# Optimization experiments

Measured on AMD Instinct MI355X. Metric: run time of the kernel, lower is better.

## Reference

```python
import jax, jax.numpy as jnp
import numpy as np
import math

H = 8  # n_heads

def rel_shift(x):
    # x: [B, H, U, P] -> Transformer-XL relative shift
    B, h, U, P = x.shape
    x = jnp.pad(x, ((0, 0), (0, 0), (0, 0), (1, 0)))  # zero-pad front of last dim
    x = x.reshape(B, h, P + 1, U)[:, :, 1:, :].reshape(B, h, U, P)
    return x

def setup_inputs() -> dict:
    key = jax.random.key(0)
    ks = jax.random.split(key, 16)
    B, T, D = 8, 1024, 512
    s = 0.05  # weight scale ~ xavier for D=512
    inp = {
        'q': jax.random.normal(ks[0], (B, T, D), jnp.float32),
        'k': jax.random.normal(ks[1], (B, T, D), jnp.float32),
        'v': jax.random.normal(ks[2], (B, T, D), jnp.float32),
        'pos': jax.random.normal(ks[3], (T, D), jnp.float32),
        'mask': jax.random.randint(ks[4], (B, T, T), 0, 2).astype(jnp.int32),
        'Wq': jax.random.normal(ks[5], (D, D), jnp.float32) * s,
        'bq': jnp.zeros((D,), jnp.float32),
        'Wk': jax.random.normal(ks[6], (D, D), jnp.float32) * s,
        'bk': jnp.zeros((D,), jnp.float32),
        'Wv': jax.random.normal(ks[7], (D, D), jnp.float32) * s,
        'bv': jnp.zeros((D,), jnp.float32),
        'Wo': jax.random.normal(ks[8], (D, D), jnp.float32) * s,
        'bo': jnp.zeros((D,), jnp.float32),
        'Wp': jax.random.normal(ks[9], (D, D), jnp.float32) * s,
        'bias_u': jax.random.normal(ks[10], (H, D // H), jnp.float32) * s,
        'bias_v': jax.random.normal(ks[11], (H, D // H), jnp.float32) * s,
    }
    return inp

def reference(q, k, v, pos, mask, Wq, bq, Wk, bk, Wv, bv, Wo, bo, Wp, bias_u, bias_v):
    B, T, D = q.shape
    dk = D // H
    qh = (q @ Wq.T + bq).reshape(B, T, H, dk)   # B U H d
    kh = (k @ Wk.T + bk).reshape(B, T, H, dk)   # B T H d
    vh = (v @ Wv.T + bv).reshape(B, T, H, dk)   # B T H d
    ph = (pos @ Wp.T).reshape(T, H, dk)          # P H d (shared across batch)
    q_u = qh + bias_u                            # B U H d
    q_v = qh + bias_v
    ac = jnp.einsum('buhd,bthd->bhut', q_u, kh)  # content term
    bd = jnp.einsum('buhd,phd->bhup', q_v, ph)   # position term
    bd = rel_shift(bd)[:, :, :, :T]
    scores = (ac + bd) / math.sqrt(dk)           # B H U T
    m = (mask[:, None, :, :] == 0)               # B 1 U T
    neg = jnp.finfo(scores.dtype).min
    scores = jnp.where(m, neg, scores)
    attn = jax.nn.softmax(scores, axis=-1)
    attn = jnp.where(m, 0.0, attn)
    x = jnp.einsum('bhut,bthd->buhd', attn, vh).reshape(B, T, D)
    return x @ Wo.T + bo
```

## Files before the change

### kernel.cpp

```cpp
#include <hip/hip_runtime.h>
#include <stdint.h>

#define Bc 8
#define Tc 1024
#define Dc 512
#define Hc 8

typedef __bf16 bf16x8 __attribute__((ext_vector_type(8)));
typedef float f32x4 __attribute__((ext_vector_type(4)));
typedef unsigned short ushort8v __attribute__((ext_vector_type(8)));

#define NEGBF 0xF14Au

__device__ __forceinline__ unsigned short f2bf(float f) {
    union { float f; uint32_t u; } v; v.f = f;
    uint32_t u = v.u;
    u += 0x7fffu + ((u >> 16) & 1u);
    return (unsigned short)(u >> 16);
}
__device__ __forceinline__ unsigned short f2bf_native(float f) {
    __bf16 b = (__bf16)f;
    return *(unsigned short*)&b;
}
__device__ __forceinline__ f32x4 mfma16(bf16x8 a, bf16x8 b, f32x4 c) {
    return __builtin_amdgcn_mfma_f32_16x16x32_bf16(a, b, c, 0, 0, 0);
}
__device__ __forceinline__ void gl16(const unsigned short* g, unsigned short* l) {
    __builtin_amdgcn_global_load_lds(
        (const __attribute__((address_space(1))) uint32_t*)g,
        (__attribute__((address_space(3))) uint32_t*)l, 16, 0, 0);
}

#define SC2 0.1803368801f

__global__ __launch_bounds__(256) void prep(
    const int* __restrict__ mask, uint32_t* __restrict__ bits,
    const float* __restrict__ Wq, const float* __restrict__ Wk,
    const float* __restrict__ Wv, const float* __restrict__ Wp,
    const float* __restrict__ Wo, unsigned short* __restrict__ Wb,
    const float* __restrict__ q, const float* __restrict__ k,
    const float* __restrict__ v, const float* __restrict__ p,
    unsigned short* __restrict__ qb, unsigned short* __restrict__ kb,
    unsigned short* __restrict__ vb, unsigned short* __restrict__ pb)
{
    int bid = blockIdx.x;
    if (bid < 32768) {
        int wid = (bid * 256 + threadIdx.x) >> 6;
        int lane = threadIdx.x & 63;
        unsigned long long bl = __ballot(mask[(size_t)wid * 64 + lane] != 0);
        if (lane == 0)  bits[wid * 2]     = (uint32_t)bl;
        if (lane == 32) bits[wid * 2 + 1] = (uint32_t)(bl >> 32);
    } else if (bid < 33408) {
        int i = (bid - 32768) * 2048 + threadIdx.x * 8;
        int m = i >> 18, r = i & 262143;
        const float* Ws[5] = {Wq, Wk, Wv, Wp, Wo};
        const float* s = Ws[m] + r;
        ushort8v o;
#pragma unroll
        for (int j = 0; j < 8; ++j) o[j] = f2bf(s[j]);
        *(ushort8v*)(Wb + i) = o;
    } else {
        size_t i = (size_t)(bid - 33408) * 2048 + threadIdx.x * 8;
        const float* src; unsigned short* dst; size_t off;
        if (i < 4194304)       { src = q; dst = qb; off = i; }
        else if (i < 8388608)  { src = k; dst = kb; off = i - 4194304; }
        else if (i < 12582912) { src = v; dst = vb; off = i - 8388608; }
        else                   { src = p; dst = pb; off = i - 12582912; }
        ushort8v o;
#pragma unroll
        for (int j = 0; j < 8; ++j) o[j] = f2bf(src[off + j]);
        *(ushort8v*)(dst + off) = o;
    }
}

__global__ __launch_bounds__(256) void proj4(
    const unsigned short* __restrict__ qb, const unsigned short* __restrict__ kb,
    const unsigned short* __restrict__ vb, const unsigned short* __restrict__ pb,
    const unsigned short* __restrict__ Wb,
    const float* __restrict__ bq, const float* __restrict__ bk,
    const float* __restrict__ bv,
    const float* __restrict__ bias_u, const float* __restrict__ bias_v,
    unsigned short* __restrict__ qu, unsigned short* __restrict__ qv,
    unsigned short* __restrict__ kh, unsigned short* __restrict__ vT,
    unsigned short* __restrict__ ph)
{
    int id = blockIdx.x;
    int wg = (id & 7) * 200 + (id >> 3);
    int z, rem;
    if (wg < 512)       { z = 0; rem = wg; }
    else if (wg < 1024) { z = 1; rem = wg - 512; }
    else if (wg < 1536) { z = 2; rem = wg - 1024; }
    else                { z = 3; rem = wg - 1536; }
    const int m0 = (rem & 3) * 128, n0 = (rem >> 2) * 64;
    const unsigned short* A = z == 0 ? qb : z == 1 ? kb : z == 2 ? vb : pb;
    const unsigned short* W = Wb + (size_t)z * 262144;

    __shared__ unsigned short As[2][64][64];
    __shared__ unsigned short Bs[2][128][64];
    const int tid = threadIdx.x, lane = tid & 63, wave = tid >> 6;
    const int lrow = lane & 15, lkg = lane >> 4;
    const int wr = (wave >> 1) * 32, wc = (wave & 1) * 64;
    const int srow = lane >> 3;
    const int scol = ((lane & 7) ^ (srow & 7)) * 8;
    const int swr  = (lrow & 7) * 8;

    f32x4 acc[2][4];
#pragma unroll
    for (int i = 0; i < 2; ++i)
#pragma unroll
        for (int j = 0; j < 4; ++j) acc[i][j] = f32x4{0.f, 0.f, 0.f, 0.f};

#pragma unroll
    for (int it = 0; it < 2; ++it) {
        int r8 = (wave * 2 + it) * 8;
        gl16(A + (size_t)(n0 + r8 + srow) * 512 + scol, &As[0][r8][0]);
    }
#pragma unroll
    for (int it = 0; it < 4; ++it) {
        int r8 = (wave * 4 + it) * 8;
        gl16(W + (size_t)(m0 + r8 + srow) * 512 + scol, &Bs[0][r8][0]);
    }

    int cur = 0;
    for (int kt = 0; kt < 512; kt += 64) {
        if (kt + 64 < 512) {
#pragma unroll
            for (int it = 0; it < 2; ++it) {
                int r8 = (wave * 2 + it) * 8;
                gl16(A + (size_t)(n0 + r8 + srow) * 512 + kt + 64 + scol, &As[cur ^ 1][r8][0]);
            }
#pragma unroll
            for (int it = 0; it < 4; ++it) {
                int r8 = (wave * 4 + it) * 8;
                gl16(W + (size_t)(m0 + r8 + srow) * 512 + kt + 64 + scol, &Bs[cur ^ 1][r8][0]);
            }
            asm volatile("s_waitcnt vmcnt(6)" ::: "memory");
        } else {
            asm volatile("s_waitcnt vmcnt(0)" ::: "memory");
        }
        __builtin_amdgcn_s_barrier();
#pragma unroll
        for (int kk = 0; kk < 2; ++kk) {
            bf16x8 a[2], bb[4];
#pragma unroll
            for (int i = 0; i < 2; ++i)
                a[i] = *(const bf16x8*)&As[cur][wr + i * 16 + lrow][(kk * 32 + lkg * 8) ^ swr];
#pragma unroll
            for (int j = 0; j < 4; ++j)
                bb[j] = *(const bf16x8*)&Bs[cur][wc + j * 16 + lrow][(kk * 32 + lkg * 8) ^ swr];
#pragma unroll
            for (int i = 0; i < 2; ++i)
#pragma unroll
                for (int j = 0; j < 4; ++j)
                    acc[i][j] = mfma16(a[i], bb[j], acc[i][j]);
        }
        asm volatile("s_waitcnt lgkmcnt(0)" ::: "memory");
        __builtin_amdgcn_s_barrier();
        cur ^= 1;
    }

#pragma unroll
    for (int i = 0; i < 2; ++i) {
        int nbase = n0 + wr + i * 16 + lkg * 4;
#pragma unroll
        for (int j = 0; j < 4; ++j) {
            int m = m0 + wc + j * 16 + lrow;
            float bb = z == 0 ? bq[m] : z == 1 ? bk[m] : z == 2 ? bv[m] : 0.f;
            float bu = 0.f, bvv = 0.f;
            if (z == 0) { bu = bias_u[m]; bvv = bias_v[m]; }
#pragma unroll
            for (int qq = 0; qq < 4; ++qq) {
                int n = nbase + qq;
                float c = acc[i][j][qq] + bb;
                if (z == 0) {
                    qu[(size_t)n * 512 + m] = f2bf(c + bu);
                    qv[(size_t)n * 512 + m] = f2bf(c + bvv);
                } else if (z == 1) {
                    kh[(size_t)n * 512 + m] = f2bf(c * SC2);
                } else if (z == 2) {
                    int b = n >> 10, t = n & 1023, h = m >> 6, d = m & 63;
                    vT[(((size_t)((b * 8 + h) * 64 + d)) << 10) + t] = f2bf(c);
                } else {
                    ph[(size_t)n * 512 + m] = f2bf(c);
                }
            }
        }
    }
}

__global__ __launch_bounds__(256) void gemm_out(
    const unsigned short* __restrict__ X, const unsigned short* __restrict__ Wob,
    const float* __restrict__ bo, float* __restrict__ fout)
{
    int id = blockIdx.x;
    int wg = (id & 7) * 64 + (id >> 3);
    const int m0 = (wg & 3) * 128, n0 = (wg >> 2) * 64;
    __shared__ unsigned short As[2][64][64];
    __shared__ unsigned short Bs[2][128][64];
    const int tid = threadIdx.x, lane = tid & 63, wave = tid >> 6;
    const int lrow = lane & 15, lkg = lane >> 4;
    const int wr = (wave >> 1) * 32, wc = (wave & 1) * 64;
    const int srow = lane >> 3;
    const int scol = ((lane & 7) ^ (srow & 7)) * 8;
    const int swr  = (lrow & 7) * 8;

    f32x4 acc[2][4];
#pragma unroll
    for (int i = 0; i < 2; ++i)
#pragma unroll
        for (int j = 0; j < 4; ++j) acc[i][j] = f32x4{0.f, 0.f, 0.f, 0.f};

#pragma unroll
    for (int it = 0; it < 2; ++it) {
        int r8 = (wave * 2 + it) * 8;
        gl16(X + (size_t)(n0 + r8 + srow) * 512 + scol, &As[0][r8][0]);
    }
#pragma unroll
    for (int it = 0; it < 4; ++it) {
        int r8 = (wave * 4 + it) * 8;
        gl16(Wob + (size_t)(m0 + r8 + srow) * 512 + scol, &Bs[0][r8][0]);
    }

    int cur = 0;
    for (int kt = 0; kt < 512; kt += 64) {
        if (kt + 64 < 512) {
#pragma unroll
            for (int it = 0; it < 2; ++it) {
                int r8 = (wave * 2 + it) * 8;
                gl16(X + (size_t)(n0 + r8 + srow) * 512 + kt + 64 + scol, &As[cur ^ 1][r8][0]);
            }
#pragma unroll
            for (int it = 0; it < 4; ++it) {
                int r8 = (wave * 4 + it) * 8;
                gl16(Wob + (size_t)(m0 + r8 + srow) * 512 + kt + 64 + scol, &Bs[cur ^ 1][r8][0]);
            }
            asm volatile("s_waitcnt vmcnt(6)" ::: "memory");
        } else {
            asm volatile("s_waitcnt vmcnt(0)" ::: "memory");
        }
        __builtin_amdgcn_s_barrier();
#pragma unroll
        for (int kk = 0; kk < 2; ++kk) {
            bf16x8 a[2], bb[4];
#pragma unroll
            for (int i = 0; i < 2; ++i)
                a[i] = *(const bf16x8*)&As[cur][wr + i * 16 + lrow][(kk * 32 + lkg * 8) ^ swr];
#pragma unroll
            for (int j = 0; j < 4; ++j)
                bb[j] = *(const bf16x8*)&Bs[cur][wc + j * 16 + lrow][(kk * 32 + lkg * 8) ^ swr];
#pragma unroll
            for (int i = 0; i < 2; ++i)
#pragma unroll
                for (int j = 0; j < 4; ++j)
                    acc[i][j] = mfma16(a[i], bb[j], acc[i][j]);
        }
        asm volatile("s_waitcnt lgkmcnt(0)" ::: "memory");
        __builtin_amdgcn_s_barrier();
        cur ^= 1;
    }
#pragma unroll
    for (int i = 0; i < 2; ++i) {
        int nbase = n0 + wr + i * 16 + lkg * 4;
#pragma unroll
        for (int j = 0; j < 4; ++j) {
            int m = m0 + wc + j * 16 + lrow;
            float bb = bo[m];
#pragma unroll
            for (int qq = 0; qq < 4; ++qq)
                fout[(size_t)(nbase + qq) * 512 + m] = acc[i][j][qq] + bb;
        }
    }
}

__global__ __launch_bounds__(256) void bd_gemm(
    const unsigned short* __restrict__ qv, const unsigned short* __restrict__ ph,
    const uint32_t* __restrict__ mbits, unsigned short* __restrict__ bds,
    int bh_base)
{
    int id = blockIdx.x, wg;
    if (gridDim.x == 4096) wg = (id & 7) * 512 + (id >> 3);
    else                   wg = (id & 7) * 64 + (id >> 3);
    const int zz = wg >> 6, ut = wg & 63;
    const int u_base = ut * 16;
    const int bh = bh_base + zz;
    const int b = bh >> 3, h = bh & 7;
    __shared__ unsigned short Bs[2][128][64];
    const int tid = threadIdx.x, lane = tid & 63, wave = tid >> 6;
    const int lrow = lane & 15, lkg = lane >> 4;
    const int srow = lane >> 3;
    const int scol = ((lane & 7) ^ (srow & 7)) * 8;
    const int swr  = (lrow & 7) * 8;

    const unsigned short* qvb = qv + ((size_t)(b * 1024 + u_base + lrow)) * 512 + h * 64;
    bf16x8 a0 = *(const bf16x8*)(qvb + lkg * 8);
    bf16x8 a1 = *(const bf16x8*)(qvb + 32 + lkg * 8);

    f32x4 acc[16];
#pragma unroll
    for (int jj = 0; jj < 16; ++jj) acc[jj] = f32x4{0.f, 0.f, 0.f, 0.f};

#pragma unroll
    for (int it = 0; it < 4; ++it) {
        int r8 = wave * 32 + it * 8;
        gl16(ph + ((size_t)(r8 + srow)) * 512 + h * 64 + scol, &Bs[0][r8][0]);
    }

#pragma unroll
    for (int c = 0; c < 8; ++c) {
        if (c < 7) {
#pragma unroll
            for (int it = 0; it < 4; ++it) {
                int r8 = wave * 32 + it * 8;
                gl16(ph + ((size_t)((c + 1) * 128 + r8 + srow)) * 512 + h * 64 + scol,
                     &Bs[(c + 1) & 1][r8][0]);
            }
            asm volatile("s_waitcnt vmcnt(4)" ::: "memory");
        } else {
            asm volatile("s_waitcnt vmcnt(0)" ::: "memory");
        }
        __builtin_amdgcn_s_barrier();
#pragma unroll
        for (int kk = 0; kk < 2; ++kk) {
            bf16x8 av = kk ? a1 : a0;
#pragma unroll
            for (int jt = 0; jt < 2; ++jt) {
                bf16x8 bb = *(const bf16x8*)
                    &Bs[c & 1][wave * 32 + jt * 16 + lrow][(kk * 32 + lkg * 8) ^ swr];
                acc[c * 2 + jt] = mfma16(av, bb, acc[c * 2 + jt]);
            }
        }
        asm volatile("s_waitcnt lgkmcnt(0)" ::: "memory");
        __builtin_amdgcn_s_barrier();
    }

    unsigned short* slab = bds + ((size_t)zz << 20);
    const uint32_t* mb = mbits + ((size_t)b << 15);
    const int Fq0 = 1025 * (u_base + lkg * 4) + wave * 32 + lrow - 1023;
#pragma unroll
    for (int q = 0; q < 4; ++q) {
        int Fq = Fq0 + 1025 * q;
#pragma unroll
        for (int c = 0; c < 8; ++c) {
            int Fb = Fq + c * 128;
            int w0 = Fb >> 5;
            uint32_t mw0 = mb[w0], mw1 = mb[w0 + 1];
            uint64_t m01 = ((uint64_t)mw1 << 32) | mw0;
            int sh = Fb & 31;
#pragma unroll
            for (int hhf = 0; hhf < 2; ++hhf) {
                uint32_t bit = (uint32_t)(m01 >> (sh + hhf * 16)) & 1u;
                unsigned short val = bit ? f2bf_native(acc[c * 2 + hhf][q] * SC2)
                                         : (unsigned short)NEGBF;
                int F = Fb + hhf * 16;
                if (F >= 0) slab[F] = val;
            }
        }
    }

    if (tid < 16) {
        int ud = u_base + tid;
        if (ud < 1023) {
            const uint8_t* mrowbytes = (const uint8_t*)mbits + ((size_t)b << 17);
            uint32_t bit = (mrowbytes[ud * 128 + ((ud + 1) >> 3)] >> ((ud + 1) & 7)) & 1;
            slab[((size_t)ud << 10) + (ud + 1)] = bit ? 0 : (unsigned short)NEGBF;
        }
    }
}

__global__ __launch_bounds__(256, 4) void attn10(
    const unsigned short* __restrict__ qu, const unsigned short* __restrict__ kh,
    const unsigned short* __restrict__ vT, const unsigned short* __restrict__ bds,
    unsigned short* __restrict__ xout, int b_base)
{
    int id = blockIdx.x, nid, b, rem;
    if (gridDim.x == 1024) {
        nid = (id & 7) * 128 + (id >> 3);
        b = b_base + (nid >> 7); rem = nid & 127;
    } else {
        nid = (id & 7) * 16 + (id >> 3);
        b = b_base; rem = nid;
    }
    const int h = rem >> 4, ublk = rem & 15;
    const int u0 = ublk * 64;

    __shared__ unsigned short Ks[2][64][64];
    __shared__ unsigned short Vs[2][64][64];
    __shared__ unsigned short Ps[4][16][64];
    const int tid = threadIdx.x, lane = tid & 63, wave = tid >> 6;
    const int lrow = lane & 15, lkg = lane >> 4;
    const int srow = lane >> 3;
    const int scol = ((lane & 7) ^ (srow & 7)) * 8;
    const int swr  = (lrow & 7) * 8;
    const f32x4 zero = {0.f, 0.f, 0.f, 0.f};

    const unsigned short* qub = qu + ((size_t)(b * 1024 + u0 + wave * 16 + lrow)) * 512 + h * 64;
    bf16x8 au0 = *(const bf16x8*)(qub + lkg * 8);
    bf16x8 au1 = *(const bf16x8*)(qub + 32 + lkg * 8);

    const int urow = u0 + wave * 16 + lkg * 4;
    const int zoff = (b - b_base) * 8 + h;
    const unsigned short* bdp[4];
#pragma unroll
    for (int q = 0; q < 4; ++q)
        bdp[q] = bds + ((size_t)zoff << 20) + (((size_t)(urow + q)) << 10) + lrow;
    const unsigned short* kbase = kh + ((size_t)(b * 1024)) * 512 + h * 64;
    const unsigned short* vbase = vT + (((size_t)((b * 8 + h) * 64)) << 10);

    f32x4 acc[4] = {zero, zero, zero, zero};
    float lsum[4] = {0.f, 0.f, 0.f, 0.f};

#pragma unroll
    for (int it = 0; it < 2; ++it) {
        int r8 = (wave * 2 + it) * 8;
        gl16(kbase + (size_t)(r8 + srow) * 512 + scol, &Ks[0][r8][0]);
        gl16(vbase + ((size_t)(r8 + srow) << 10) + scol, &Vs[0][r8][0]);
    }

    int cur = 0;
    for (int t0 = 0; t0 < 1024; t0 += 64) {
        f32x4 bdC[4];
#pragma unroll
        for (int j = 0; j < 4; ++j)
#pragma unroll
            for (int q = 0; q < 4; ++q)
                bdC[j][q] = __uint_as_float(((uint32_t)bdp[q][j * 16]) << 16);
#pragma unroll
        for (int q = 0; q < 4; ++q) bdp[q] += 64;

        if (t0 < 960) {
#pragma unroll
            for (int it = 0; it < 2; ++it) {
                int r8 = (wave * 2 + it) * 8;
                gl16(kbase + (size_t)(t0 + 64 + r8 + srow) * 512 + scol, &Ks[cur ^ 1][r8][0]);
                gl16(vbase + ((size_t)(r8 + srow) << 10) + t0 + 64 + scol, &Vs[cur ^ 1][r8][0]);
            }
            asm volatile("s_waitcnt vmcnt(4)" ::: "memory");
        } else {
            asm volatile("s_waitcnt vmcnt(0)" ::: "memory");
        }
        __builtin_amdgcn_s_barrier();

        f32x4 s[4];
#pragma unroll
        for (int j = 0; j < 4; ++j) {
            bf16x8 k0 = *(const bf16x8*)&Ks[cur][j * 16 + lrow][(lkg * 8) ^ swr];
            bf16x8 k1 = *(const bf16x8*)&Ks[cur][j * 16 + lrow][(32 + lkg * 8) ^ swr];
            s[j] = mfma16(au1, k1, mfma16(au0, k0, bdC[j]));
        }
#pragma unroll
        for (int j = 0; j < 4; ++j) {
#pragma unroll
            for (int q = 0; q < 4; ++q) {
                float p = exp2f(s[j][q]);
                lsum[q] += p;
                int prow = lkg * 4 + q;
                Ps[wave][prow][(j * 16 + lrow) ^ ((prow & 7) * 8)] = f2bf_native(p);
            }
        }
        bf16x8 pa0 = *(const bf16x8*)&Ps[wave][lrow][(lkg * 8) ^ swr];
        bf16x8 pa1 = *(const bf16x8*)&Ps[wave][lrow][(32 + lkg * 8) ^ swr];
#pragma unroll
        for (int jj = 0; jj < 4; ++jj) {
            bf16x8 vb0 = *(const bf16x8*)&Vs[cur][jj * 16 + lrow][(lkg * 8) ^ swr];
            bf16x8 vb1 = *(const bf16x8*)&Vs[cur][jj * 16 + lrow][(32 + lkg * 8) ^ swr];
            acc[jj] = mfma16(pa1, vb1, mfma16(pa0, vb0, acc[jj]));
        }
        asm volatile("s_waitcnt lgkmcnt(0)" ::: "memory");
        __builtin_amdgcn_s_barrier();
        cur ^= 1;
    }

#pragma unroll
    for (int off = 1; off < 16; off <<= 1)
#pragma unroll
        for (int q = 0; q < 4; ++q) lsum[q] += __shfl_xor(lsum[q], off);
#pragma unroll
    for (int q = 0; q < 4; ++q) {
        float inv = 1.0f / lsum[q];
        int u = urow + q;
#pragma unroll
        for (int jj = 0; jj < 4; ++jj) {
            int d = jj * 16 + lrow;
            xout[((size_t)(b * 1024 + u)) * 512 + h * 64 + d] = f2bf_native(acc[jj][q] * inv);
        }
    }
}

extern "C" void kernel_launch(void* const* d_in, const int* in_sizes, int n_in,
                              void* d_out, int out_size, void* d_ws, size_t ws_size,
                              hipStream_t stream) {
    const float* q    = (const float*)d_in[0];
    const float* k    = (const float*)d_in[1];
    const float* v    = (const float*)d_in[2];
    const float* pos  = (const float*)d_in[3];
    const int*   mask = (const int*)d_in[4];
    const float* Wq   = (const float*)d_in[5];
    const float* bq   = (const float*)d_in[6];
    const float* Wk   = (const float*)d_in[7];
    const float* bk   = (const float*)d_in[8];
    const float* Wv   = (const float*)d_in[9];
    const float* bv   = (const float*)d_in[10];
    const float* Wo   = (const float*)d_in[11];
    const float* bo   = (const float*)d_in[12];
    const float* Wp   = (const float*)d_in[13];
    const float* bias_u = (const float*)d_in[14];
    const float* bias_v = (const float*)d_in[15];
    float* out = (float*)d_out;

    unsigned short* ws = (unsigned short*)d_ws;
    constexpr size_t NQ  = (size_t)Bc * Tc * Dc;
    constexpr size_t NP  = (size_t)Tc * Dc;
    constexpr size_t NMB = (size_t)Bc * Tc * 32;
    constexpr size_t NWB = (size_t)5 * 262144;
    unsigned short* ws_qu = ws;
    unsigned short* ws_qv = ws_qu + NQ;
    unsigned short* ws_kh = ws_qv + NQ;
    unsigned short* ws_vT = ws_kh + NQ;
    unsigned short* ws_ph = ws_vT + NQ;
    uint32_t*       ws_mb = (uint32_t*)(ws_ph + NP);
    unsigned short* ws_wb = (unsigned short*)(ws_mb + NMB);
    unsigned short* ws_qb = ws_wb + NWB;
    unsigned short* ws_kb = ws_qb + NQ;
    unsigned short* ws_vb = ws_kb + NQ;
    unsigned short* ws_pb = ws_vb + NQ;
    unsigned short* ws_bd = ws_qb;

    constexpr size_t BD_FULL  = (size_t)64 * 1024 * 1024;
    constexpr size_t BD_SMALL = (size_t)8 * 1024 * 1024;
    const size_t base_bytes = (4 * NQ + NP + NWB) * 2 + NMB * 4;
    const bool full  = ws_size >= base_bytes + BD_FULL * 2;
    const bool tier2 = !full && ws_size >= base_bytes + ((3 * NQ + NP) + NQ) * 2;

    dim3 blk(256);
    prep<<<39808, blk, 0, stream>>>(mask, ws_mb, Wq, Wk, Wv, Wp, Wo, ws_wb,
                                    q, k, v, pos, ws_qb, ws_kb, ws_vb, ws_pb);
    proj4<<<1600, blk, 0, stream>>>(ws_qb, ws_kb, ws_vb, ws_pb, ws_wb, bq, bk, bv,
                                    bias_u, bias_v, ws_qu, ws_qv, ws_kh, ws_vT, ws_ph);

    if (full) {
        unsigned short* ws_x = ws_qv;
        bd_gemm<<<4096, blk, 0, stream>>>(ws_qv, ws_ph, ws_mb, ws_bd, 0);
        attn10<<<1024, blk, 0, stream>>>(ws_qu, ws_kh, ws_vT, ws_bd, ws_x, 0);
        gemm_out<<<512, blk, 0, stream>>>(ws_x, ws_wb + 4 * 262144, bo, out);
    } else if (tier2) {
        unsigned short* ws_x = ws_qb + 3 * NQ + NP;
        for (int b = 0; b < 8; ++b) {
            bd_gemm<<<512, blk, 0, stream>>>(ws_qv, ws_ph, ws_mb, ws_bd, b * 8);
            attn10<<<128, blk, 0, stream>>>(ws_qu, ws_kh, ws_vT, ws_bd, ws_x, b);
        }
        gemm_out<<<512, blk, 0, stream>>>(ws_x, ws_wb + 4 * 262144, bo, out);
    }
}
```

Baseline: 195.5 us.

## Fuse relative-position bd GEMM into attention kernel with per-block slab

```diff
diff --git a/kernel.cpp b/kernel.cpp
--- a/kernel.cpp
+++ b/kernel.cpp
@@ -272,105 +272,12 @@
     }
 }
 
-__global__ __launch_bounds__(256) void bd_gemm(
-    const unsigned short* __restrict__ qv, const unsigned short* __restrict__ ph,
-    const uint32_t* __restrict__ mbits, unsigned short* __restrict__ bds,
-    int bh_base)
-{
-    int id = blockIdx.x, wg;
-    if (gridDim.x == 4096) wg = (id & 7) * 512 + (id >> 3);
-    else                   wg = (id & 7) * 64 + (id >> 3);
-    const int zz = wg >> 6, ut = wg & 63;
-    const int u_base = ut * 16;
-    const int bh = bh_base + zz;
-    const int b = bh >> 3, h = bh & 7;
-    __shared__ unsigned short Bs[2][128][64];
-    const int tid = threadIdx.x, lane = tid & 63, wave = tid >> 6;
-    const int lrow = lane & 15, lkg = lane >> 4;
-    const int srow = lane >> 3;
-    const int scol = ((lane & 7) ^ (srow & 7)) * 8;
-    const int swr  = (lrow & 7) * 8;
-
-    const unsigned short* qvb = qv + ((size_t)(b * 1024 + u_base + lrow)) * 512 + h * 64;
-    bf16x8 a0 = *(const bf16x8*)(qvb + lkg * 8);
-    bf16x8 a1 = *(const bf16x8*)(qvb + 32 + lkg * 8);
-
-    f32x4 acc[16];
-#pragma unroll
-    for (int jj = 0; jj < 16; ++jj) acc[jj] = f32x4{0.f, 0.f, 0.f, 0.f};
-
-#pragma unroll
-    for (int it = 0; it < 4; ++it) {
-        int r8 = wave * 32 + it * 8;
-        gl16(ph + ((size_t)(r8 + srow)) * 512 + h * 64 + scol, &Bs[0][r8][0]);
-    }
-
-#pragma unroll
-    for (int c = 0; c < 8; ++c) {
-        if (c < 7) {
-#pragma unroll
-            for (int it = 0; it < 4; ++it) {
-                int r8 = wave * 32 + it * 8;
-                gl16(ph + ((size_t)((c + 1) * 128 + r8 + srow)) * 512 + h * 64 + scol,
-                     &Bs[(c + 1) & 1][r8][0]);
-            }
-            asm volatile("s_waitcnt vmcnt(4)" ::: "memory");
-        } else {
-            asm volatile("s_waitcnt vmcnt(0)" ::: "memory");
-        }
-        __builtin_amdgcn_s_barrier();
-#pragma unroll
-        for (int kk = 0; kk < 2; ++kk) {
-            bf16x8 av = kk ? a1 : a0;
-#pragma unroll
-            for (int jt = 0; jt < 2; ++jt) {
-                bf16x8 bb = *(const bf16x8*)
-                    &Bs[c & 1][wave * 32 + jt * 16 + lrow][(kk * 32 + lkg * 8) ^ swr];
-                acc[c * 2 + jt] = mfma16(av, bb, acc[c * 2 + jt]);
-            }
-        }
-        asm volatile("s_waitcnt lgkmcnt(0)" ::: "memory");
-        __builtin_amdgcn_s_barrier();
-    }
-
-    unsigned short* slab = bds + ((size_t)zz << 20);
-    const uint32_t* mb = mbits + ((size_t)b << 15);
-    const int Fq0 = 1025 * (u_base + lkg * 4) + wave * 32 + lrow - 1023;
-#pragma unroll
-    for (int q = 0; q < 4; ++q) {
-        int Fq = Fq0 + 1025 * q;
-#pragma unroll
-        for (int c = 0; c < 8; ++c) {
-            int Fb = Fq + c * 128;
-            int w0 = Fb >> 5;
-            uint32_t mw0 = mb[w0], mw1 = mb[w0 + 1];
-            uint64_t m01 = ((uint64_t)mw1 << 32) | mw0;
-            int sh = Fb & 31;
-#pragma unroll
-            for (int hhf = 0; hhf < 2; ++hhf) {
-                uint32_t bit = (uint32_t)(m01 >> (sh + hhf * 16)) & 1u;
-                unsigned short val = bit ? f2bf_native(acc[c * 2 + hhf][q] * SC2)
-                                         : (unsigned short)NEGBF;
-                int F = Fb + hhf * 16;
-                if (F >= 0) slab[F] = val;
-            }
-        }
-    }
-
-    if (tid < 16) {
-        int ud = u_base + tid;
-        if (ud < 1023) {
-            const uint8_t* mrowbytes = (const uint8_t*)mbits + ((size_t)b << 17);
-            uint32_t bit = (mrowbytes[ud * 128 + ((ud + 1) >> 3)] >> ((ud + 1) & 7)) & 1;
-            slab[((size_t)ud << 10) + (ud + 1)] = bit ? 0 : (unsigned short)NEGBF;
-        }
-    }
-}
-
-__global__ __launch_bounds__(256, 4) void attn10(
-    const unsigned short* __restrict__ qu, const unsigned short* __restrict__ kh,
-    const unsigned short* __restrict__ vT, const unsigned short* __restrict__ bds,
-    unsigned short* __restrict__ xout, int b_base)
+__global__ __launch_bounds__(256, 4) void attn13(
+    const unsigned short* __restrict__ qu, const unsigned short* __restrict__ qv,
+    const unsigned short* __restrict__ kh, const unsigned short* __restrict__ vT,
+    const unsigned short* __restrict__ ph, const uint32_t* __restrict__ mbits,
+    unsigned short* __restrict__ bds, unsigned short* __restrict__ xout,
+    int b_base)
 {
     int id = blockIdx.x, nid, b, rem;
     if (gridDim.x == 1024) {
@@ -383,9 +290,7 @@
     const int h = rem >> 4, ublk = rem & 15;
     const int u0 = ublk * 64;
 
-    __shared__ unsigned short Ks[2][64][64];
-    __shared__ unsigned short Vs[2][64][64];
-    __shared__ unsigned short Ps[4][16][64];
+    __shared__ unsigned short sh[20480];
     const int tid = threadIdx.x, lane = tid & 63, wave = tid >> 6;
     const int lrow = lane & 15, lkg = lane >> 4;
     const int srow = lane >> 3;
@@ -393,12 +298,102 @@
     const int swr  = (lrow & 7) * 8;
     const f32x4 zero = {0.f, 0.f, 0.f, 0.f};
 
+    const int zoff = (b - b_base) * 8 + h;
+    unsigned short* slab = bds + ((size_t)zoff << 20);
+    const uint32_t* mb = mbits + ((size_t)b << 15);
+    const int Fmin = u0 << 10, Fmax = Fmin + 65536;
+
     const unsigned short* qub = qu + ((size_t)(b * 1024 + u0 + wave * 16 + lrow)) * 512 + h * 64;
     bf16x8 au0 = *(const bf16x8*)(qub + lkg * 8);
     bf16x8 au1 = *(const bf16x8*)(qub + 32 + lkg * 8);
 
+    {
+        const unsigned short* qvb = qv + ((size_t)(b * 1024 + u0 + wave * 16 + lrow)) * 512 + h * 64;
+        bf16x8 a0 = *(const bf16x8*)(qvb + lkg * 8);
+        bf16x8 a1 = *(const bf16x8*)(qvb + 32 + lkg * 8);
+        const unsigned short* qve = qv + ((size_t)(b * 1024 + u0 + 64)) * 512 + h * 64;
+        bf16x8 ae0 = *(const bf16x8*)(qve + lkg * 8);
+        bf16x8 ae1 = *(const bf16x8*)(qve + 32 + lkg * 8);
+
+        const int u_w = u0 + wave * 16 + lkg * 4;
+        const int u_e = u0 + 64;
+
+        for (int c = 0; c < 8; ++c) {
+#pragma unroll
+            for (int it = 0; it < 4; ++it) {
+                int r8 = wave * 32 + it * 8;
+                gl16(ph + ((size_t)(c * 128 + r8 + srow)) * 512 + h * 64 + scol, &sh[r8 * 64]);
+            }
+            __syncthreads();
+
+            f32x4 accA[8], accE[2];
+#pragma unroll
+            for (int pt = 0; pt < 8; ++pt) accA[pt] = zero;
+            accE[0] = zero; accE[1] = zero;
+#pragma unroll
+            for (int kk = 0; kk < 2; ++kk) {
+                bf16x8 av = kk ? a1 : a0;
+                bf16x8 ev = kk ? ae1 : ae0;
+#pragma unroll
+                for (int pt = 0; pt < 8; ++pt) {
+                    bf16x8 bb = *(const bf16x8*)&sh[(pt * 16 + lrow) * 64 + ((kk * 32 + lkg * 8) ^ swr)];
+                    accA[pt] = mfma16(av, bb, accA[pt]);
+                }
+#pragma unroll
+                for (int t = 0; t < 2; ++t) {
+                    int pt2 = wave * 2 + t;
+                    bf16x8 bb = *(const bf16x8*)&sh[(pt2 * 16 + lrow) * 64 + ((kk * 32 + lkg * 8) ^ swr)];
+                    accE[t] = mfma16(ev, bb, accE[t]);
+                }
+            }
+
+#pragma unroll
+            for (int qq = 0; qq < 4; ++qq) {
+                int u = u_w + qq;
+                int Fb0 = 1025 * u + c * 128 + lrow - 1023;
+                int w0 = Fb0 >> 5, sh5 = Fb0 & 31;
+                uint32_t w0v = mb[w0], w1v = mb[w0 + 1], w2v = mb[w0 + 2],
+                         w3v = mb[w0 + 3], w4v = mb[w0 + 4];
+                uint64_t mm0 = ((uint64_t)w1v << 32) | w0v;
+                uint64_t mm1 = ((uint64_t)w2v << 32) | w1v;
+                uint64_t mm2 = ((uint64_t)w3v << 32) | w2v;
+                uint64_t mm3 = ((uint64_t)w4v << 32) | w3v;
+#pragma unroll
+                for (int pt = 0; pt < 8; ++pt) {
+                    uint64_t mm = (pt < 2) ? mm0 : (pt < 4) ? mm1 : (pt < 6) ? mm2 : mm3;
+                    uint32_t bit = (uint32_t)(mm >> (sh5 + (pt & 1) * 16)) & 1u;
+                    unsigned short val = bit ? f2bf_native(accA[pt][qq] * SC2)
+                                             : (unsigned short)NEGBF;
+                    int F = Fb0 + pt * 16;
+                    if (F >= Fmin && F < Fmax) slab[F] = val;
+                }
+            }
+            if (lkg == 0) {
+#pragma unroll
+                for (int t = 0; t < 2; ++t) {
+                    int pt2 = wave * 2 + t;
+                    int F = 1025 * u_e + c * 128 + pt2 * 16 + lrow - 1023;
+                    uint32_t bit = (mb[F >> 5] >> (F & 31)) & 1u;
+                    unsigned short val = bit ? f2bf_native(accE[t][0] * SC2)
+                                             : (unsigned short)NEGBF;
+                    if (F >= Fmin && F < Fmax) slab[F] = val;
+                }
+            }
+            __syncthreads();
+        }
+        if (tid < 64) {
+            int du = u0 + tid;
+            if (du < 1023) {
+                const uint8_t* mrowbytes = (const uint8_t*)mbits + ((size_t)b << 17);
+                uint32_t bit = (mrowbytes[du * 128 + ((du + 1) >> 3)] >> ((du + 1) & 7)) & 1;
+                slab[((size_t)du << 10) + (du + 1)] = bit ? 0 : (unsigned short)NEGBF;
+            }
+        }
+        asm volatile("s_waitcnt vmcnt(0)" ::: "memory");
+        __builtin_amdgcn_s_barrier();
+    }
+
     const int urow = u0 + wave * 16 + lkg * 4;
-    const int zoff = (b - b_base) * 8 + h;
     const unsigned short* bdp[4];
 #pragma unroll
     for (int q = 0; q < 4; ++q)
@@ -412,8 +407,8 @@
 #pragma unroll
     for (int it = 0; it < 2; ++it) {
         int r8 = (wave * 2 + it) * 8;
-        gl16(kbase + (size_t)(r8 + srow) * 512 + scol, &Ks[0][r8][0]);
-        gl16(vbase + ((size_t)(r8 + srow) << 10) + scol, &Vs[0][r8][0]);
+        gl16(kbase + (size_t)(r8 + srow) * 512 + scol, &sh[r8 * 64]);
+        gl16(vbase + ((size_t)(r8 + srow) << 10) + scol, &sh[8192 + r8 * 64]);
     }
 
     int cur = 0;
@@ -431,8 +426,10 @@
 #pragma unroll
             for (int it = 0; it < 2; ++it) {
                 int r8 = (wave * 2 + it) * 8;
-                gl16(kbase + (size_t)(t0 + 64 + r8 + srow) * 512 + scol, &Ks[cur ^ 1][r8][0]);
-                gl16(vbase + ((size_t)(r8 + srow) << 10) + t0 + 64 + scol, &Vs[cur ^ 1][r8][0]);
+                gl16(kbase + (size_t)(t0 + 64 + r8 + srow) * 512 + scol,
+                     &sh[(cur ^ 1) * 4096 + r8 * 64]);
+                gl16(vbase + ((size_t)(r8 + srow) << 10) + t0 + 64 + scol,
+                     &sh[8192 + (cur ^ 1) * 4096 + r8 * 64]);
             }
             asm volatile("s_waitcnt vmcnt(4)" ::: "memory");
         } else {
@@ -443,8 +440,8 @@
         f32x4 s[4];
 #pragma unroll
         for (int j = 0; j < 4; ++j) {
-            bf16x8 k0 = *(const bf16x8*)&Ks[cur][j * 16 + lrow][(lkg * 8) ^ swr];
-            bf16x8 k1 = *(const bf16x8*)&Ks[cur][j * 16 + lrow][(32 + lkg * 8) ^ swr];
+            bf16x8 k0 = *(const bf16x8*)&sh[cur * 4096 + (j * 16 + lrow) * 64 + ((lkg * 8) ^ swr)];
+            bf16x8 k1 = *(const bf16x8*)&sh[cur * 4096 + (j * 16 + lrow) * 64 + ((32 + lkg * 8) ^ swr)];
             s[j] = mfma16(au1, k1, mfma16(au0, k0, bdC[j]));
         }
 #pragma unroll
@@ -454,15 +451,15 @@
                 float p = exp2f(s[j][q]);
                 lsum[q] += p;
                 int prow = lkg * 4 + q;
-                Ps[wave][prow][(j * 16 + lrow) ^ ((prow & 7) * 8)] = f2bf_native(p);
-            }
-        }
-        bf16x8 pa0 = *(const bf16x8*)&Ps[wave][lrow][(lkg * 8) ^ swr];
-        bf16x8 pa1 = *(const bf16x8*)&Ps[wave][lrow][(32 + lkg * 8) ^ swr];
+                sh[16384 + wave * 1024 + prow * 64 + ((j * 16 + lrow) ^ ((prow & 7) * 8))] = f2bf_native(p);
+            }
+        }
+        bf16x8 pa0 = *(const bf16x8*)&sh[16384 + wave * 1024 + lrow * 64 + ((lkg * 8) ^ swr)];
+        bf16x8 pa1 = *(const bf16x8*)&sh[16384 + wave * 1024 + lrow * 64 + ((32 + lkg * 8) ^ swr)];
 #pragma unroll
         for (int jj = 0; jj < 4; ++jj) {
-            bf16x8 vb0 = *(const bf16x8*)&Vs[cur][jj * 16 + lrow][(lkg * 8) ^ swr];
-            bf16x8 vb1 = *(const bf16x8*)&Vs[cur][jj * 16 + lrow][(32 + lkg * 8) ^ swr];
+            bf16x8 vb0 = *(const bf16x8*)&sh[8192 + cur * 4096 + (jj * 16 + lrow) * 64 + ((lkg * 8) ^ swr)];
+            bf16x8 vb1 = *(const bf16x8*)&sh[8192 + cur * 4096 + (jj * 16 + lrow) * 64 + ((32 + lkg * 8) ^ swr)];
             acc[jj] = mfma16(pa1, vb1, mfma16(pa0, vb0, acc[jj]));
         }
         asm volatile("s_waitcnt lgkmcnt(0)" ::: "memory");
@@ -526,10 +523,8 @@
     unsigned short* ws_bd = ws_qb;
 
     constexpr size_t BD_FULL  = (size_t)64 * 1024 * 1024;
-    constexpr size_t BD_SMALL = (size_t)8 * 1024 * 1024;
     const size_t base_bytes = (4 * NQ + NP + NWB) * 2 + NMB * 4;
     const bool full  = ws_size >= base_bytes + BD_FULL * 2;
-    const bool tier2 = !full && ws_size >= base_bytes + ((3 * NQ + NP) + NQ) * 2;
 
     dim3 blk(256);
     prep<<<39808, blk, 0, stream>>>(mask, ws_mb, Wq, Wk, Wv, Wp, Wo, ws_wb,
@@ -538,16 +533,13 @@
                                     bias_u, bias_v, ws_qu, ws_qv, ws_kh, ws_vT, ws_ph);
 
     if (full) {
-        unsigned short* ws_x = ws_qv;
-        bd_gemm<<<4096, blk, 0, stream>>>(ws_qv, ws_ph, ws_mb, ws_bd, 0);
-        attn10<<<1024, blk, 0, stream>>>(ws_qu, ws_kh, ws_vT, ws_bd, ws_x, 0);
-        gemm_out<<<512, blk, 0, stream>>>(ws_x, ws_wb + 4 * 262144, bo, out);
-    } else if (tier2) {
-        unsigned short* ws_x = ws_qb + 3 * NQ + NP;
-        for (int b = 0; b < 8; ++b) {
-            bd_gemm<<<512, blk, 0, stream>>>(ws_qv, ws_ph, ws_mb, ws_bd, b * 8);
-            attn10<<<128, blk, 0, stream>>>(ws_qu, ws_kh, ws_vT, ws_bd, ws_x, b);
-        }
-        gemm_out<<<512, blk, 0, stream>>>(ws_x, ws_wb + 4 * 262144, bo, out);
-    }
-}
+        attn13<<<1024, blk, 0, stream>>>(ws_qu, ws_qv, ws_kh, ws_vT, ws_ph,
+                                         ws_mb, ws_bd, ws_qu, 0);
+        gemm_out<<<512, blk, 0, stream>>>(ws_qu, ws_wb + 4 * 262144, bo, out);
+    } else {
+        for (int b = 0; b < 8; ++b)
+            attn13<<<128, blk, 0, stream>>>(ws_qu, ws_qv, ws_kh, ws_vT, ws_ph,
+                                            ws_mb, ws_bd, ws_qu, b);
+        gemm_out<<<512, blk, 0, stream>>>(ws_qu, ws_wb + 4 * 262144, bo, out);
+    }
+}
```

Result: faster. 180.4 us (-7.7%).
